# Kernel optimization log

Measured on AMD Instinct MI355X. Metric: run time of the kernel, lower is better.

Reference implementation:

```python
import jax, jax.numpy as jnp
import numpy as np


def setup_inputs() -> dict:
    key = jax.random.key(0)
    k1, k2, k3, k4 = jax.random.split(key, 4)
    B, C, H, W = 8, 3, 1024, 2048
    M, h, w = 32, H // 8, W // 8
    img = jax.random.uniform(k1, (B, C, H, W), dtype=jnp.float32)
    planar_masks = jax.random.normal(k2, (B, M, h, w), dtype=jnp.float32)
    disp = jax.random.uniform(k3, (B, h, w), dtype=jnp.float32) * 0.9 + 0.1
    K = jnp.array([[721.5, 0.0, w / 2.0], [0.0, 721.5, h / 2.0], [0.0, 0.0, 1.0]], dtype=jnp.float32)
    intrs = jnp.tile(K[None], (B, 1, 1))
    baseline = jax.random.uniform(k4, (B,), dtype=jnp.float32) * 0.4 + 0.3
    return {"img": img, "planar_masks": planar_masks, "disp": disp, "intrs": intrs, "baseline": baseline}


def reference(img, planar_masks, disp, intrs, baseline):
    B, C, H, W = img.shape
    _, M, h, w = planar_masks.shape
    dt = img.dtype

    # disp -> depth (b,h,w)
    focal = (intrs[:, 0, 0] + intrs[:, 1, 1]) * 0.5
    depth = baseline[:, None, None] * focal[:, None, None] / (disp * 2048.0)

    # depth -> normals via 3x3 Sobel-style central differences, zero padding
    dp = jnp.pad(depth, ((0, 0), (1, 1), (1, 1)))
    gx = 0.5 * (dp[:, 1:-1, 2:] - dp[:, 1:-1, :-2])
    gy = 0.5 * (dp[:, 2:, 1:-1] - dp[:, :-2, 1:-1])
    dir_map = jnp.stack([-gx, -gy, jnp.ones_like(gx)], axis=1)  # (B,3,h,w)
    normal = dir_map / jnp.sqrt(jnp.sum(dir_map ** 2, axis=1, keepdims=True))

    # softmax-weighted per-plane depth/normal (faithful torch .view memory layout)
    wts = jax.nn.softmax(planar_masks.reshape(B, M, h * w), axis=-1)  # (B,M,hw)
    flat_depth = depth.reshape(B, h * w, 1)
    flat_normal = normal.reshape(B, h * w, 3)  # channel-major flatten, as in source
    planar_depth = wts @ flat_depth   # (B,M,1)
    planar_normal = wts @ flat_normal  # (B,M,3)

    # per-plane homographies H = K (R - t n^T / d) K^-1
    R = jnp.broadcast_to(jnp.eye(3, dtype=dt), (B, 3, 3))
    t = jnp.zeros((B, 3, 1), dt).at[:, 2, 0].set(-baseline)
    K_inv = jnp.linalg.inv(intrs)
    tn = t[:, None] @ planar_normal[:, :, None, :]            # (B,M,3,3)
    H_cal = R[:, None] - tn / planar_depth[..., None]
    Hm = intrs[:, None] @ H_cal @ K_inv[:, None]              # (B,M,3,3)

    img_p = img.reshape(B, C, h, 8, w, 8).mean(axis=(3, 5))  # (B,C,h,w)

    # affine_grid (align_corners=True) with the top 2 rows of H
    ys = jnp.linspace(-1.0, 1.0, h, dtype=dt)
    xs = jnp.linspace(-1.0, 1.0, w, dtype=dt)
    gyy, gxx = jnp.meshgrid(ys, xs, indexing="ij")
    base = jnp.stack([gxx, gyy, jnp.ones_like(gxx)], axis=-1)  # (h,w,3)
    grid = jnp.einsum("bmij,hwj->bmhwi", Hm[:, :, :2, :], base)  # (B,M,h,w,2)

    # bilinear grid_sample, zeros padding, align_corners=True
    ix = (grid[..., 0] + 1.0) * (w - 1) * 0.5
    iy = (grid[..., 1] + 1.0) * (h - 1) * 0.5
    x0 = jnp.floor(ix)
    y0 = jnp.floor(iy)
    wx1 = ix - x0
    wy1 = iy - y0
    imgT = img_p.transpose(0, 2, 3, 1)  # (B,h,w,C)
    bidx = jnp.arange(B)[:, None, None, None]

    def corner(xf, yf):
        valid = (xf >= 0) & (xf <= w - 1) & (yf >= 0) & (yf <= h - 1)
        xi = jnp.clip(xf, 0, w - 1).astype(jnp.int32)
        yi = jnp.clip(yf, 0, h - 1).astype(jnp.int32)
        return imgT[bidx, yi, xi] * valid[..., None].astype(dt)  # (B,M,h,w,C)

    warp = (corner(x0, y0) * ((1 - wx1) * (1 - wy1))[..., None]
            + corner(x0 + 1, y0) * (wx1 * (1 - wy1))[..., None]
            + corner(x0, y0 + 1) * ((1 - wx1) * wy1)[..., None]
            + corner(x0 + 1, y0 + 1) * (wx1 * wy1)[..., None])  # (B,M,h,w,C)

    blend = jax.nn.softmax(planar_masks, axis=1)  # (B,M,h,w)
    return jnp.einsum("bmhwc,bmhw->bchw", warp, blend)
```

## Files before the change

### kernel.cpp

```cpp
#include <hip/hip_runtime.h>
#include <math.h>

#define Bq   8
#define Cc   3
#define Hh   128
#define Ww   256
#define Mm   32
#define HW   (Hh*Ww)
#define HIMG 1024
#define WIMG 2048

typedef float f32x4 __attribute__((ext_vector_type(4)));

__global__ void k_dn(const float* __restrict__ disp,
                     const float* __restrict__ intrs,
                     const float* __restrict__ baseline,
                     float* __restrict__ depth,
                     float* __restrict__ normal) {
    int idx = blockIdx.x * 256 + threadIdx.x;
    int b = idx >> 15;
    int p = idx & (HW - 1);
    int y = p >> 8;
    int x = p & (Ww - 1);
    float focal = 0.5f * (intrs[b * 9 + 0] + intrs[b * 9 + 4]);
    float k = baseline[b] * focal * (1.0f / 2048.0f);
    const float* db = disp + (size_t)b * HW;
    float Dc  = k / db[p];
    float Dxm = (x > 0)      ? k / db[p - 1]  : 0.0f;
    float Dxp = (x < Ww - 1) ? k / db[p + 1]  : 0.0f;
    float Dym = (y > 0)      ? k / db[p - Ww] : 0.0f;
    float Dyp = (y < Hh - 1) ? k / db[p + Ww] : 0.0f;
    float gx = 0.5f * (Dxp - Dxm);
    float gy = 0.5f * (Dyp - Dym);
    float invn = 1.0f / sqrtf(gx * gx + gy * gy + 1.0f);
    depth[idx] = Dc;
    float* nb = normal + (size_t)b * 3 * HW;
    nb[p]          = -gx * invn;
    nb[HW + p]     = -gy * invn;
    nb[2 * HW + p] =  invn;
}

__global__ __launch_bounds__(512) void k_pool_planes(
        const float* __restrict__ img, float4* __restrict__ img_p,
        const float* __restrict__ masks,
        const float* __restrict__ depth, const float* __restrict__ normal,
        const float* __restrict__ intrs, const float* __restrict__ baseline,
        float* __restrict__ hm) {
    int blk = blockIdx.x;
    int tid = threadIdx.x;
    __shared__ float lds[5][8];
    if (blk < Bq * Mm) {
        int bm = blk;
        int b = bm >> 5;
        const float4* mp = (const float4*)(masks + (size_t)bm * HW);
        const float4* dp = (const float4*)(depth + (size_t)b * HW);
        const float4* np = (const float4*)(normal + (size_t)b * 3 * HW);
        int lane = tid & 63, wid = tid >> 6;

        float se = 0.f, sd = 0.f, s0 = 0.f, s1 = 0.f, s2 = 0.f;
        #pragma unroll 4
        for (int kk = 0; kk < HW / 4 / 512; kk++) {
            int i = tid + kk * 512;
            float4 mk  = mp[i];
            float4 d4  = dp[i];
            float4 n0v = np[3 * i], n1v = np[3 * i + 1], n2v = np[3 * i + 2];
            float e0 = __expf(mk.x), e1 = __expf(mk.y);
            float e2 = __expf(mk.z), e3 = __expf(mk.w);
            se += (e0 + e1) + (e2 + e3);
            sd = fmaf(e0, d4.x, fmaf(e1, d4.y, fmaf(e2, d4.z, fmaf(e3, d4.w, sd))));
            s0 = fmaf(e0, n0v.x, fmaf(e1, n0v.w, fmaf(e2, n1v.z, fmaf(e3, n2v.y, s0))));
            s1 = fmaf(e0, n0v.y, fmaf(e1, n1v.x, fmaf(e2, n1v.w, fmaf(e3, n2v.z, s1))));
            s2 = fmaf(e0, n0v.z, fmaf(e1, n1v.y, fmaf(e2, n2v.x, fmaf(e3, n2v.w, s2))));
        }
        float vals[5] = {se, sd, s0, s1, s2};
        #pragma unroll
        for (int j = 0; j < 5; j++) {
            float v = vals[j];
            #pragma unroll
            for (int off = 32; off; off >>= 1) v += __shfl_down(v, off, 64);
            if (lane == 0) lds[j][wid] = v;
        }
        __syncthreads();

        if (tid == 0) {
            float t[5];
            #pragma unroll
            for (int j = 0; j < 5; j++) {
                float r = 0.f;
                #pragma unroll
                for (int i = 0; i < 8; i++) r += lds[j][i];
                t[j] = r;
            }
            float inv_se = 1.0f / t[0];
            float pd = t[1] * inv_se;
            float n0 = t[2] * inv_se, n1 = t[3] * inv_se, n2 = t[4] * inv_se;
            const float* Km = intrs + b * 9;
            float a = Km[0], bb = Km[1], c = Km[2];
            float d = Km[3], e  = Km[4], f = Km[5];
            float g = Km[6], h2 = Km[7], i = Km[8];
            float det = a * (e * i - f * h2) - bb * (d * i - f * g) + c * (d * h2 - e * g);
            float invd = 1.0f / det;
            float ki[9] = {(e * i - f * h2) * invd, (c * h2 - bb * i) * invd, (bb * f - c * e) * invd,
                           (f * g - d * i) * invd, (a * i - c * g) * invd,  (c * d - a * f) * invd,
                           (d * h2 - e * g) * invd, (bb * g - a * h2) * invd, (a * e - bb * d) * invd};
            float s = baseline[b] / pd;
            float A[9] = {1.f, 0.f, 0.f, 0.f, 1.f, 0.f, s * n0, s * n1, 1.0f + s * n2};
            float T[9];
            #pragma unroll
            for (int r = 0; r < 3; r++)
                #pragma unroll
                for (int cc = 0; cc < 3; cc++)
                    T[r * 3 + cc] = Km[r * 3 + 0] * A[cc] + Km[r * 3 + 1] * A[3 + cc] + Km[r * 3 + 2] * A[6 + cc];
            #pragma unroll
            for (int r = 0; r < 2; r++)
                #pragma unroll
                for (int cc = 0; cc < 3; cc++)
                    hm[bm * 6 + r * 3 + cc] = T[r * 3 + 0] * ki[cc] + T[r * 3 + 1] * ki[3 + cc] + T[r * 3 + 2] * ki[6 + cc];
        }
    } else {
        int pb = blk - Bq * Mm;
        int b = pb >> 6;
        int y = ((pb & 63) << 1) | (tid >> 8);
        int x = tid & 255;
        float s[3];
        #pragma unroll
        for (int c = 0; c < 3; c++) {
            const float* base = img + ((size_t)(b * 3 + c) * HIMG + (size_t)y * 8) * WIMG + x * 8;
            float acc = 0.f;
            #pragma unroll
            for (int r = 0; r < 8; r++) {
                f32x4 u = __builtin_nontemporal_load((const f32x4*)(base + (size_t)r * WIMG));
                f32x4 v = __builtin_nontemporal_load((const f32x4*)(base + (size_t)r * WIMG + 4));
                acc += u.x + u.y + u.z + u.w + v.x + v.y + v.z + v.w;
            }
            s[c] = acc * (1.0f / 64.0f);
        }
        img_p[((size_t)(b * Hh + y)) * Ww + x] = make_float4(s[0], s[1], s[2], 0.f);
    }
}

__global__ __launch_bounds__(256) void k_blend(const float* __restrict__ masks,
                        const float* __restrict__ hm,
                        const float4* __restrict__ img_p,
                        float* __restrict__ out) {
    int blk = blockIdx.x;
    int b = blk >> 6;
    int y0 = (blk & 63) << 1;
    int x = threadIdx.x;
    __shared__ float hs[Mm * 6];
    if (x < Mm * 6) hs[x] = hm[b * Mm * 6 + x];
    __syncthreads();

    const float* mp = masks + (size_t)b * Mm * HW + (size_t)y0 * Ww + x;
    float xn  = (2.0f * x - (float)(Ww - 1)) * (1.0f / (float)(Ww - 1));
    float yn0 = (2.0f * y0 - (float)(Hh - 1)) * (1.0f / (float)(Hh - 1));
    float yn1 = (2.0f * (y0 + 1) - (float)(Hh - 1)) * (1.0f / (float)(Hh - 1));
    const float4* ip = img_p + (size_t)b * HW;

    float se0 = 0.f, a00 = 0.f, a01 = 0.f, a02 = 0.f;
    float se1 = 0.f, a10 = 0.f, a11 = 0.f, a12 = 0.f;
    #pragma unroll 4
    for (int m = 0; m < Mm; m++) {
        float mv0 = mp[(size_t)m * HW];
        float mv1 = mp[(size_t)m * HW + Ww];
        float e0 = __expf(mv0);
        float e1 = __expf(mv1);
        se0 += e0;
        se1 += e1;
        float h0 = hs[m * 6 + 0], h1 = hs[m * 6 + 1], h2 = hs[m * 6 + 2];
        float h3 = hs[m * 6 + 3], h4 = hs[m * 6 + 4], h5 = hs[m * 6 + 5];
        #define ROWSAMPLE(YN, E, SA0, SA1, SA2) do {                                \
            float gx = fmaf(h0, xn, fmaf(h1, (YN), h2));                            \
            float gy = fmaf(h3, xn, fmaf(h4, (YN), h5));                            \
            float ix = (gx + 1.0f) * ((float)(Ww - 1) * 0.5f);                      \
            float iy = (gy + 1.0f) * ((float)(Hh - 1) * 0.5f);                      \
            float x0f = floorf(ix), y0f = floorf(iy);                               \
            float wx1 = ix - x0f, wy1 = iy - y0f;                                   \
            float wx0 = 1.0f - wx1, wy0 = 1.0f - wy1;                               \
            int x0i = (int)x0f, y0i = (int)y0f;                                     \
            float vx0 = ((unsigned)x0i       < (unsigned)Ww) ? wx0 : 0.0f;          \
            float vx1 = ((unsigned)(x0i + 1) < (unsigned)Ww) ? wx1 : 0.0f;          \
            float vy0 = ((unsigned)y0i       < (unsigned)Hh) ? wy0 * (E) : 0.0f;    \
            float vy1 = ((unsigned)(y0i + 1) < (unsigned)Hh) ? wy1 * (E) : 0.0f;    \
            int xc0 = min(max(x0i, 0), Ww - 1);                                     \
            int xc1 = min(max(x0i + 1, 0), Ww - 1);                                 \
            int r0 = min(max(y0i, 0), Hh - 1) * Ww;                                 \
            int r1 = min(max(y0i + 1, 0), Hh - 1) * Ww;                             \
            float4 t00 = ip[r0 + xc0];                                              \
            float4 t10 = ip[r0 + xc1];                                              \
            float4 t01 = ip[r1 + xc0];                                              \
            float4 t11 = ip[r1 + xc1];                                              \
            float w00 = vx0 * vy0, w10 = vx1 * vy0;                                 \
            float w01 = vx0 * vy1, w11 = vx1 * vy1;                                 \
            SA0 = fmaf(w00, t00.x, fmaf(w10, t10.x, fmaf(w01, t01.x, fmaf(w11, t11.x, SA0)))); \
            SA1 = fmaf(w00, t00.y, fmaf(w10, t10.y, fmaf(w01, t01.y, fmaf(w11, t11.y, SA1)))); \
            SA2 = fmaf(w00, t00.z, fmaf(w10, t10.z, fmaf(w01, t01.z, fmaf(w11, t11.z, SA2)))); \
        } while (0)
        ROWSAMPLE(yn0, e0, a00, a01, a02);
        ROWSAMPLE(yn1, e1, a10, a11, a12);
        #undef ROWSAMPLE
    }
    int o = y0 * Ww + x;
    float* ob = out + (size_t)b * 3 * HW;
    float inv0 = 1.0f / se0;
    ob[o]          = a00 * inv0;
    ob[HW + o]     = a01 * inv0;
    ob[2 * HW + o] = a02 * inv0;
    float inv1 = 1.0f / se1;
    ob[o + Ww]          = a10 * inv1;
    ob[HW + o + Ww]     = a11 * inv1;
    ob[2 * HW + o + Ww] = a12 * inv1;
}

extern "C" void kernel_launch(void* const* d_in, const int* in_sizes, int n_in,
                              void* d_out, int out_size, void* d_ws, size_t ws_size,
                              hipStream_t stream) {
    const float* img      = (const float*)d_in[0];
    const float* masks    = (const float*)d_in[1];
    const float* disp     = (const float*)d_in[2];
    const float* intrs    = (const float*)d_in[3];
    const float* baseline = (const float*)d_in[4];
    float* out = (float*)d_out;

    float* depth  = (float*)d_ws;
    float* normal = depth + (size_t)Bq * HW;
    float* hm     = normal + (size_t)Bq * 3 * HW;
    float4* img_p = (float4*)(hm + (size_t)Bq * Mm * 6);

    hipLaunchKernelGGL(k_dn, dim3(Bq * Hh), dim3(256), 0, stream,
                       disp, intrs, baseline, depth, normal);
    hipLaunchKernelGGL(k_pool_planes, dim3(Bq * Mm + Bq * Hh / 2), dim3(512), 0, stream,
                       img, img_p, masks, depth, normal, intrs, baseline, hm);
    hipLaunchKernelGGL(k_blend, dim3(Bq * Hh / 2), dim3(256), 0, stream,
                       masks, hm, img_p, out);
}
```

Baseline: 330.8 us.

## Split image pooling across first two kernels to overlap with depth/normal work

Moves half of the 8x average-pool work into the depth/normal kernel, so the bandwidth-heavy image reads overlap with the small depth computation, and the rest stays beside the plane-reduction blocks. The depth/normal kernel now covers two pixels per thread across 256 blocks. The final output stores become nontemporal so they don't pollute the cache. This rebalances work between kernels to cut idle time in the short first kernel. It risks uneven block durations within each combined launch.

```diff
diff --git a/kernel.cpp b/kernel.cpp
--- a/kernel.cpp
+++ b/kernel.cpp
@@ -12,32 +12,64 @@
 
 typedef float f32x4 __attribute__((ext_vector_type(4)));
 
-__global__ void k_dn(const float* __restrict__ disp,
-                     const float* __restrict__ intrs,
-                     const float* __restrict__ baseline,
-                     float* __restrict__ depth,
-                     float* __restrict__ normal) {
-    int idx = blockIdx.x * 256 + threadIdx.x;
-    int b = idx >> 15;
-    int p = idx & (HW - 1);
-    int y = p >> 8;
-    int x = p & (Ww - 1);
-    float focal = 0.5f * (intrs[b * 9 + 0] + intrs[b * 9 + 4]);
-    float k = baseline[b] * focal * (1.0f / 2048.0f);
-    const float* db = disp + (size_t)b * HW;
-    float Dc  = k / db[p];
-    float Dxm = (x > 0)      ? k / db[p - 1]  : 0.0f;
-    float Dxp = (x < Ww - 1) ? k / db[p + 1]  : 0.0f;
-    float Dym = (y > 0)      ? k / db[p - Ww] : 0.0f;
-    float Dyp = (y < Hh - 1) ? k / db[p + Ww] : 0.0f;
-    float gx = 0.5f * (Dxp - Dxm);
-    float gy = 0.5f * (Dyp - Dym);
-    float invn = 1.0f / sqrtf(gx * gx + gy * gy + 1.0f);
-    depth[idx] = Dc;
-    float* nb = normal + (size_t)b * 3 * HW;
-    nb[p]          = -gx * invn;
-    nb[HW + p]     = -gy * invn;
-    nb[2 * HW + p] =  invn;
+__device__ __forceinline__ void pool_pair(const float* __restrict__ img,
+                                          float4* __restrict__ img_p,
+                                          int pair, int tid) {
+    int b = pair >> 6;
+    int y = ((pair & 63) << 1) | (tid >> 8);
+    int x = tid & 255;
+    float s[3];
+    #pragma unroll
+    for (int c = 0; c < 3; c++) {
+        const float* base = img + ((size_t)(b * 3 + c) * HIMG + (size_t)y * 8) * WIMG + x * 8;
+        float acc = 0.f;
+        #pragma unroll
+        for (int r = 0; r < 8; r++) {
+            f32x4 u = __builtin_nontemporal_load((const f32x4*)(base + (size_t)r * WIMG));
+            f32x4 v = __builtin_nontemporal_load((const f32x4*)(base + (size_t)r * WIMG + 4));
+            acc += u.x + u.y + u.z + u.w + v.x + v.y + v.z + v.w;
+        }
+        s[c] = acc * (1.0f / 64.0f);
+    }
+    img_p[((size_t)(b * Hh + y)) * Ww + x] = make_float4(s[0], s[1], s[2], 0.f);
+}
+
+__global__ __launch_bounds__(512) void k_dn_pool(
+        const float* __restrict__ img, float4* __restrict__ img_p,
+        const float* __restrict__ disp,
+        const float* __restrict__ intrs, const float* __restrict__ baseline,
+        float* __restrict__ depth, float* __restrict__ normal) {
+    int blk = blockIdx.x;
+    int tid = threadIdx.x;
+    if (blk < 256) {
+        int t = blk * 512 + tid;
+        #pragma unroll
+        for (int j = 0; j < 2; j++) {
+            int idx = t + j * 131072;
+            int b = idx >> 15;
+            int p = idx & (HW - 1);
+            int y = p >> 8;
+            int x = p & (Ww - 1);
+            float focal = 0.5f * (intrs[b * 9 + 0] + intrs[b * 9 + 4]);
+            float k = baseline[b] * focal * (1.0f / 2048.0f);
+            const float* db = disp + (size_t)b * HW;
+            float Dc  = k / db[p];
+            float Dxm = (x > 0)      ? k / db[p - 1]  : 0.0f;
+            float Dxp = (x < Ww - 1) ? k / db[p + 1]  : 0.0f;
+            float Dym = (y > 0)      ? k / db[p - Ww] : 0.0f;
+            float Dyp = (y < Hh - 1) ? k / db[p + Ww] : 0.0f;
+            float gx = 0.5f * (Dxp - Dxm);
+            float gy = 0.5f * (Dyp - Dym);
+            float invn = 1.0f / sqrtf(gx * gx + gy * gy + 1.0f);
+            depth[idx] = Dc;
+            float* nb = normal + (size_t)b * 3 * HW;
+            nb[p]          = -gx * invn;
+            nb[HW + p]     = -gy * invn;
+            nb[2 * HW + p] =  invn;
+        }
+    } else {
+        pool_pair(img, img_p, (blk - 256) * 2, tid);
+    }
 }
 
 __global__ __launch_bounds__(512) void k_pool_planes(
@@ -118,24 +150,7 @@
                     hm[bm * 6 + r * 3 + cc] = T[r * 3 + 0] * ki[cc] + T[r * 3 + 1] * ki[3 + cc] + T[r * 3 + 2] * ki[6 + cc];
         }
     } else {
-        int pb = blk - Bq * Mm;
-        int b = pb >> 6;
-        int y = ((pb & 63) << 1) | (tid >> 8);
-        int x = tid & 255;
-        float s[3];
-        #pragma unroll
-        for (int c = 0; c < 3; c++) {
-            const float* base = img + ((size_t)(b * 3 + c) * HIMG + (size_t)y * 8) * WIMG + x * 8;
-            float acc = 0.f;
-            #pragma unroll
-            for (int r = 0; r < 8; r++) {
-                f32x4 u = __builtin_nontemporal_load((const f32x4*)(base + (size_t)r * WIMG));
-                f32x4 v = __builtin_nontemporal_load((const f32x4*)(base + (size_t)r * WIMG + 4));
-                acc += u.x + u.y + u.z + u.w + v.x + v.y + v.z + v.w;
-            }
-            s[c] = acc * (1.0f / 64.0f);
-        }
-        img_p[((size_t)(b * Hh + y)) * Ww + x] = make_float4(s[0], s[1], s[2], 0.f);
+        pool_pair(img, img_p, (blk - 256) * 2 + 1, tid);
     }
 }
 
@@ -203,13 +218,13 @@
     int o = y0 * Ww + x;
     float* ob = out + (size_t)b * 3 * HW;
     float inv0 = 1.0f / se0;
-    ob[o]          = a00 * inv0;
-    ob[HW + o]     = a01 * inv0;
-    ob[2 * HW + o] = a02 * inv0;
     float inv1 = 1.0f / se1;
-    ob[o + Ww]          = a10 * inv1;
-    ob[HW + o + Ww]     = a11 * inv1;
-    ob[2 * HW + o + Ww] = a12 * inv1;
+    __builtin_nontemporal_store(a00 * inv0, ob + o);
+    __builtin_nontemporal_store(a01 * inv0, ob + HW + o);
+    __builtin_nontemporal_store(a02 * inv0, ob + 2 * HW + o);
+    __builtin_nontemporal_store(a10 * inv1, ob + o + Ww);
+    __builtin_nontemporal_store(a11 * inv1, ob + HW + o + Ww);
+    __builtin_nontemporal_store(a12 * inv1, ob + 2 * HW + o + Ww);
 }
 
 extern "C" void kernel_launch(void* const* d_in, const int* in_sizes, int n_in,
@@ -227,9 +242,9 @@
     float* hm     = normal + (size_t)Bq * 3 * HW;
     float4* img_p = (float4*)(hm + (size_t)Bq * Mm * 6);
 
-    hipLaunchKernelGGL(k_dn, dim3(Bq * Hh), dim3(256), 0, stream,
-                       disp, intrs, baseline, depth, normal);
-    hipLaunchKernelGGL(k_pool_planes, dim3(Bq * Mm + Bq * Hh / 2), dim3(512), 0, stream,
+    hipLaunchKernelGGL(k_dn_pool, dim3(512), dim3(512), 0, stream,
+                       img, img_p, disp, intrs, baseline, depth, normal);
+    hipLaunchKernelGGL(k_pool_planes, dim3(512), dim3(512), 0, stream,
                        img, img_p, masks, depth, normal, intrs, baseline, hm);
     hipLaunchKernelGGL(k_blend, dim3(Bq * Hh / 2), dim3(256), 0, stream,
                        masks, hm, img_p, out);
```

New measurement: 329.5 us. No clear change (-0.4%).
